# Kernel optimization log

Measured on AMD Instinct MI355X. Metric: run time of the kernel, lower is better.

## Reference

```python
import jax, jax.numpy as jnp
import numpy as np

B = 32768
N_TABLES = 26
N_ROWS = 200000
D = 64
N_DENSE = 13
NUM_PAIRS = (N_TABLES + 1) * N_TABLES // 2  # 351, pairs j < i over 27 vectors


def setup_inputs() -> dict:
    key = jax.random.key(0)
    ks = jax.random.split(key, 16)
    def lin(kw, kb, m, n):
        W = jax.random.normal(kw, (m, n), jnp.float32) * np.sqrt(2.0 / (m + n))
        b = jax.random.normal(kb, (m,), jnp.float32) * np.sqrt(1.0 / m)
        return W, b
    bw0, bb0 = lin(ks[0], ks[1], 512, N_DENSE)
    bw1, bb1 = lin(ks[2], ks[3], 256, 512)
    bw2, bb2 = lin(ks[4], ks[5], D, 256)
    tw0, tb0 = lin(ks[6], ks[7], 512, D + NUM_PAIRS)
    tw1, tb1 = lin(ks[8], ks[9], 256, 512)
    tw2, tb2 = lin(ks[10], ks[11], 1, 256)
    bound = np.sqrt(1.0 / N_ROWS)
    emb_tables = jax.random.uniform(ks[12], (N_TABLES, N_ROWS, D), jnp.float32,
                                    minval=-bound, maxval=bound)
    dense_x = jax.random.uniform(ks[13], (B, N_DENSE), jnp.float32)
    indices = jax.random.randint(ks[14], (N_TABLES, B), 0, N_ROWS, jnp.int64)
    return {"dense_x": dense_x, "indices": indices, "emb_tables": emb_tables,
            "bw0": bw0, "bb0": bb0, "bw1": bw1, "bb1": bb1, "bw2": bw2, "bb2": bb2,
            "tw0": tw0, "tb0": tb0, "tw1": tw1, "tb1": tb1, "tw2": tw2, "tb2": tb2}


def reference(dense_x, indices, emb_tables,
              bw0, bb0, bw1, bb1, bw2, bb2,
              tw0, tb0, tw1, tb1, tw2, tb2):
    # bottom MLP (all ReLU, sigmoid_bot = -1)
    h = jax.nn.relu(dense_x @ bw0.T + bb0)
    h = jax.nn.relu(h @ bw1.T + bb1)
    x_bot = jax.nn.relu(h @ bw2.T + bb2)          # [B, D]

    # multi-table EmbeddingBag(sum) with single-index bags -> plain gather
    embs = jax.vmap(lambda tbl, idx: tbl[idx])(emb_tables, indices)  # [26, B, D]

    # dot interaction over 27 feature vectors
    T = jnp.concatenate([x_bot[None], embs], axis=0).transpose(1, 0, 2)  # [B, 27, D]
    Z = jnp.einsum('bnd,bmd->bnm', T, T)                                 # [B, 27, 27]
    li, lj = jnp.tril_indices(N_TABLES + 1, k=-1)  # pairs with j < i (no self)
    Zflat = Z[:, li, lj]                           # [B, 351]
    R = jnp.concatenate([x_bot, Zflat], axis=1)    # [B, 415]

    # top MLP: ReLU, ReLU, Sigmoid (sigmoid_top = 2)
    h = jax.nn.relu(R @ tw0.T + tb0)
    h = jax.nn.relu(h @ tw1.T + tb1)
    p = jax.nn.sigmoid(h @ tw2.T + tb2)            # [B, 1]
    return p
```

## Files before the change

### kernel.cpp

```cpp
#include <hip/hip_runtime.h>
#include <cstddef>
#include <cstdint>

#define B_SZ    32768
#define NTAB    26
#define NROWS   200000

typedef __attribute__((ext_vector_type(8))) short short8v;
typedef __attribute__((ext_vector_type(4))) float f32x4;
typedef __attribute__((ext_vector_type(16))) float f32x16;

__device__ __forceinline__ ushort f2bf(float f) {
    uint32_t u = __builtin_bit_cast(uint32_t, f);
    u += 0x7FFFu + ((u >> 16) & 1u);
    return (ushort)(u >> 16);
}
__device__ __forceinline__ void stage16(const ushort* g, ushort* l) {
    __builtin_amdgcn_global_load_lds(
        (const __attribute__((address_space(1))) unsigned int*)g,
        (__attribute__((address_space(3))) unsigned int*)l, 16, 0, 0);
}

__global__ __launch_bounds__(256) void conv_all_k(
    const float* __restrict__ dense_x, const float* __restrict__ bw0,
    const float* __restrict__ tw0, const float* __restrict__ bw1,
    const float* __restrict__ bw2, const float* __restrict__ tw1,
    ushort* __restrict__ dense_pad, ushort* __restrict__ bw0p,
    ushort* __restrict__ tw0p, ushort* __restrict__ bw1c,
    ushort* __restrict__ bw2c, ushort* __restrict__ tw1c)
{
    const int gid = blockIdx.x * 256 + threadIdx.x;
    if (gid < 1048576) {
        int r = gid >> 5, k = gid & 31;
        dense_pad[gid] = (k < 13) ? f2bf(dense_x[r * 13 + k]) : (ushort)0;
    } else if (gid < 1064960) {
        int i = gid - 1048576; int r = i >> 5, k = i & 31;
        bw0p[i] = (k < 13) ? f2bf(bw0[r * 13 + k]) : (ushort)0;
    } else if (gid < 1277952) {
        int i = gid - 1064960; int r = i / 416, k = i - r * 416;
        tw0p[i] = (k < 415) ? f2bf(tw0[r * 415 + k]) : (ushort)0;
    } else if (gid < 1409024) {
        int i = gid - 1277952; bw1c[i] = f2bf(bw1[i]);
    } else if (gid < 1425408) {
        int i = gid - 1409024; bw2c[i] = f2bf(bw2[i]);
    } else if (gid < 1556480) {
        int i = gid - 1425408; tw1c[i] = f2bf(tw1[i]);
    }
}

__global__ __launch_bounds__(256, 2) void fused_k(
    const ushort* __restrict__ dense_pad, const ushort* __restrict__ bw0p,
    const float* __restrict__ bb0, const ushort* __restrict__ bw1c,
    const float* __restrict__ bb1, const ushort* __restrict__ bw2c,
    const float* __restrict__ bb2,
    const float* __restrict__ emb, const int* __restrict__ indices,
    const ushort* __restrict__ tw0p, const float* __restrict__ tb0,
    const ushort* __restrict__ tw1c, const float* __restrict__ tb1,
    const float* __restrict__ tw2, const float* __restrict__ tb2,
    float* __restrict__ out)
{
    __shared__ __align__(16) ushort R1[32 * 512];
    __shared__ __align__(16) ushort Wst[2][256 * 32];
    __shared__ __align__(16) ushort R3[32 * 256];
    const int t = threadIdx.x;
    const int lane = t & 63, w = t >> 6;
    const int fr = lane & 15, j16 = lane >> 4;
    const int bBase = blockIdx.x * 32;

    int ir0, ir1, ir2, ir3;
    ir0 = indices[(size_t)(t >> 5) * B_SZ + bBase + (t & 31)];
    ir1 = indices[(size_t)((256 + t) >> 5) * B_SZ + bBase + ((256 + t) & 31)];
    ir2 = indices[(size_t)((512 + t) >> 5) * B_SZ + bBase + ((512 + t) & 31)];
    ir3 = (t < 64) ? indices[(size_t)((768 + t) >> 5) * B_SZ + bBase + ((768 + t) & 31)] : 0;

    if (t < 128) {
        const int r = t >> 2, u = t & 3, us = u ^ ((r >> 1) & 3);
        stage16(dense_pad + (size_t)(bBase + r) * 32 + us * 8, &R3[t * 8]);
    }
#pragma unroll
    for (int i = 0; i < 4; ++i) {
        const int idx = i * 256 + t;
        const int r = idx >> 2, u = idx & 3, us = u ^ ((r >> 1) & 3);
        stage16(bw0p + (size_t)r * 32 + us * 8, &Wst[0][idx * 8]);
        stage16(bw0p + (size_t)(256 + r) * 32 + us * 8, &Wst[1][idx * 8]);
    }
    __syncthreads();

    f32x4 acc0[2][2][4] = {};
    {
        short8v a[2];
#pragma unroll
        for (int m = 0; m < 2; ++m) {
            const int r = m * 16 + fr;
            a[m] = *(const short8v*)&R3[r * 32 + (j16 ^ ((r >> 1) & 3)) * 8];
        }
#pragma unroll
        for (int hh = 0; hh < 2; ++hh) {
            short8v b[4];
#pragma unroll
            for (int n = 0; n < 4; ++n) {
                const int lr = w * 64 + n * 16 + fr;
                b[n] = *(const short8v*)&Wst[hh][lr * 32 + (j16 ^ ((lr >> 1) & 3)) * 8];
            }
            __builtin_amdgcn_s_setprio(1);
#pragma unroll
            for (int m = 0; m < 2; ++m)
#pragma unroll
                for (int n = 0; n < 4; ++n)
                    acc0[hh][m][n] = __builtin_amdgcn_mfma_f32_16x16x32_bf16(b[n], a[m], acc0[hh][m][n], 0, 0, 0);
            __builtin_amdgcn_s_setprio(0);
        }
    }
    __syncthreads();

#pragma unroll
    for (int i = 0; i < 4; ++i) {
        const int idx = i * 256 + t;
        const int r = idx >> 2, u = idx & 3, us = u ^ ((r >> 1) & 3);
        stage16(bw1c + (size_t)r * 512 + us * 8, &Wst[0][idx * 8]);
        stage16(bw1c + (size_t)r * 512 + 32 + us * 8, &Wst[1][idx * 8]);
    }
#pragma unroll
    for (int hh = 0; hh < 2; ++hh)
#pragma unroll
    for (int n = 0; n < 4; ++n) {
        const int ch = hh * 256 + w * 64 + n * 16 + j16 * 4;
        const float4 bv = *(const float4*)&bb0[ch];
#pragma unroll
        for (int m = 0; m < 2; ++m) {
            const int s = m * 16 + fr;
            ushort4 o;
            o.x = f2bf(fmaxf(acc0[hh][m][n][0] + bv.x, 0.f));
            o.y = f2bf(fmaxf(acc0[hh][m][n][1] + bv.y, 0.f));
            o.z = f2bf(fmaxf(acc0[hh][m][n][2] + bv.z, 0.f));
            o.w = f2bf(fmaxf(acc0[hh][m][n][3] + bv.w, 0.f));
            const int u = ch >> 3, su = u ^ (s & 7);
            *(ushort4*)&R1[s * 512 + su * 8 + (ch & 7)] = o;
        }
    }
    __syncthreads();

    f32x4 acc1[2][4] = {};
    for (int i8 = 0; i8 < 8; ++i8) {
#pragma unroll
        for (int half = 0; half < 2; ++half) {
            const int kt = i8 * 64 + half * 32;
            short8v a[2], b[4];
#pragma unroll
            for (int m = 0; m < 2; ++m) {
                const int s = m * 16 + fr;
                const int u = (kt >> 3) + j16, su = u ^ (s & 7);
                a[m] = *(const short8v*)&R1[s * 512 + su * 8];
            }
#pragma unroll
            for (int n = 0; n < 4; ++n) {
                const int lr = w * 64 + n * 16 + fr;
                b[n] = *(const short8v*)&Wst[half][lr * 32 + (j16 ^ ((lr >> 1) & 3)) * 8];
            }
            __builtin_amdgcn_s_setprio(1);
#pragma unroll
            for (int m = 0; m < 2; ++m)
#pragma unroll
                for (int n = 0; n < 4; ++n)
                    acc1[m][n] = __builtin_amdgcn_mfma_f32_16x16x32_bf16(b[n], a[m], acc1[m][n], 0, 0, 0);
            __builtin_amdgcn_s_setprio(0);
        }
        __syncthreads();
        if (i8 < 7) {
            const int kt2 = (i8 + 1) * 64;
#pragma unroll
            for (int i = 0; i < 4; ++i) {
                const int idx = i * 256 + t;
                const int r = idx >> 2, u = idx & 3, us = u ^ ((r >> 1) & 3);
                stage16(bw1c + (size_t)r * 512 + kt2 + us * 8, &Wst[0][idx * 8]);
                stage16(bw1c + (size_t)r * 512 + kt2 + 32 + us * 8, &Wst[1][idx * 8]);
            }
            __syncthreads();
        }
    }
    {
        const int r = t >> 2, u = t & 3, us = u ^ ((r >> 1) & 3);
        stage16(bw2c + (size_t)r * 256 + us * 8, &Wst[0][t * 8]);
        stage16(bw2c + (size_t)r * 256 + 32 + us * 8, &Wst[1][t * 8]);
    }
#pragma unroll
    for (int n = 0; n < 4; ++n) {
        const int ch = w * 64 + n * 16 + j16 * 4;
        const float4 bv = *(const float4*)&bb1[ch];
#pragma unroll
        for (int m = 0; m < 2; ++m) {
            const int s = m * 16 + fr;
            ushort4 o;
            o.x = f2bf(fmaxf(acc1[m][n][0] + bv.x, 0.f));
            o.y = f2bf(fmaxf(acc1[m][n][1] + bv.y, 0.f));
            o.z = f2bf(fmaxf(acc1[m][n][2] + bv.z, 0.f));
            o.w = f2bf(fmaxf(acc1[m][n][3] + bv.w, 0.f));
            const int u = ch >> 3, su = u ^ (s & 7);
            *(ushort4*)&R3[s * 256 + su * 8 + (ch & 7)] = o;
        }
    }
    __syncthreads();

    f32x4 acc2[2] = {};
    for (int i8 = 0; i8 < 4; ++i8) {
#pragma unroll
        for (int half = 0; half < 2; ++half) {
            const int kt = i8 * 64 + half * 32;
            short8v a[2], b;
#pragma unroll
            for (int m = 0; m < 2; ++m) {
                const int s = m * 16 + fr;
                const int u = (kt >> 3) + j16, su = u ^ (s & 7);
                a[m] = *(const short8v*)&R3[s * 256 + su * 8];
            }
            {
                const int lr = w * 16 + fr;
                b = *(const short8v*)&Wst[half][lr * 32 + (j16 ^ ((lr >> 1) & 3)) * 8];
            }
#pragma unroll
            for (int m = 0; m < 2; ++m)
                acc2[m] = __builtin_amdgcn_mfma_f32_16x16x32_bf16(b, a[m], acc2[m], 0, 0, 0);
        }
        __syncthreads();
        if (i8 < 3) {
            const int kt2 = (i8 + 1) * 64;
            const int r = t >> 2, u = t & 3, us = u ^ ((r >> 1) & 3);
            stage16(bw2c + (size_t)r * 256 + kt2 + us * 8, &Wst[0][t * 8]);
            stage16(bw2c + (size_t)r * 256 + kt2 + 32 + us * 8, &Wst[1][t * 8]);
            __syncthreads();
        }
    }
    {
        const int ch = w * 16 + j16 * 4;
        const float4 bv = *(const float4*)&bb2[ch];
#pragma unroll
        for (int m = 0; m < 2; ++m) {
            const int s = m * 16 + fr;
            ushort4 o;
            o.x = f2bf(fmaxf(acc2[m][0] + bv.x, 0.f));
            o.y = f2bf(fmaxf(acc2[m][1] + bv.y, 0.f));
            o.z = f2bf(fmaxf(acc2[m][2] + bv.z, 0.f));
            o.w = f2bf(fmaxf(acc2[m][3] + bv.w, 0.f));
            *(ushort4*)&R1[s * 424 + ch] = o;
        }
    }
    if (t < 32) R1[t * 424 + 415] = 0;
    {
        int* sc = (int*)R3;
        sc[t] = ir0; sc[256 + t] = ir1; sc[512 + t] = ir2;
        if (t < 64) sc[768 + t] = ir3;
    }
#pragma unroll
    for (int i = 0; i < 4; ++i) {
        const int idx = i * 256 + t;
        const int r = idx >> 2, u = idx & 3, us = u ^ ((r >> 1) & 3);
        stage16(tw0p + (size_t)r * 416 + us * 8, &Wst[0][idx * 8]);
        stage16(tw0p + (size_t)(256 + r) * 416 + us * 8, &Wst[1][idx * 8]);
    }
    __syncthreads();

    {
        const int* sc = (const int*)R3;
        const int r32 = lane & 31, half = lane >> 5;
        for (int it = 0; it < 8; ++it) {
            const int s = it * 4 + w;
            short8v tf[4];
            if (r32 == 0) {
#pragma unroll
                for (int kq = 0; kq < 4; ++kq)
                    tf[kq] = *(const short8v*)&R1[s * 424 + kq * 16 + half * 8];
            } else if (r32 <= 26) {
                const int idxv = sc[(r32 - 1) * 32 + s];
                const float* rp = emb + ((size_t)(r32 - 1) * NROWS + (size_t)idxv) * 64 + half * 8;
#pragma unroll
                for (int kq = 0; kq < 4; ++kq) {
                    const f32x4 x = *(const f32x4*)&rp[kq * 16];
                    const f32x4 y = *(const f32x4*)&rp[kq * 16 + 4];
                    short8v v;
                    v[0] = (short)f2bf(x[0]); v[1] = (short)f2bf(x[1]);
                    v[2] = (short)f2bf(x[2]); v[3] = (short)f2bf(x[3]);
                    v[4] = (short)f2bf(y[0]); v[5] = (short)f2bf(y[1]);
                    v[6] = (short)f2bf(y[2]); v[7] = (short)f2bf(y[3]);
                    tf[kq] = v;
                }
            } else {
#pragma unroll
                for (int kq = 0; kq < 4; ++kq) tf[kq] = (short8v)0;
            }
            f32x16 c = {};
#pragma unroll
            for (int kq = 0; kq < 4; ++kq)
                c = __builtin_amdgcn_mfma_f32_32x32x16_bf16(tf[kq], tf[kq], c, 0, 0, 0);
#pragma unroll
            for (int reg = 0; reg < 16; ++reg) {
                const int r = (reg & 3) + 8 * (reg >> 2) + 4 * half;
                if (r < 27 && r32 < r)
                    R1[s * 424 + 64 + (r * (r - 1)) / 2 + r32] = f2bf(c[reg]);
            }
        }
    }
    __syncthreads();

    f32x4 accA[2][2][4] = {};
    for (int kt_i = 0; kt_i < 13; ++kt_i) {
        const int kt = kt_i * 32;
        short8v a[2];
#pragma unroll
        for (int m = 0; m < 2; ++m) {
            const int s = m * 16 + fr;
            a[m] = *(const short8v*)&R1[s * 424 + ((kt >> 3) + j16) * 8];
        }
#pragma unroll
        for (int hh = 0; hh < 2; ++hh) {
            short8v b[4];
#pragma unroll
            for (int n = 0; n < 4; ++n) {
                const int lr = w * 64 + n * 16 + fr;
                b[n] = *(const short8v*)&Wst[hh][lr * 32 + (j16 ^ ((lr >> 1) & 3)) * 8];
            }
            __builtin_amdgcn_s_setprio(1);
#pragma unroll
            for (int m = 0; m < 2; ++m)
#pragma unroll
                for (int n = 0; n < 4; ++n)
                    accA[hh][m][n] = __builtin_amdgcn_mfma_f32_16x16x32_bf16(b[n], a[m], accA[hh][m][n], 0, 0, 0);
            __builtin_amdgcn_s_setprio(0);
        }
        __syncthreads();
        if (kt_i < 12) {
            const int kt2 = kt + 32;
#pragma unroll
            for (int i = 0; i < 4; ++i) {
                const int idx = i * 256 + t;
                const int r = idx >> 2, u = idx & 3, us = u ^ ((r >> 1) & 3);
                stage16(tw0p + (size_t)r * 416 + kt2 + us * 8, &Wst[0][idx * 8]);
                stage16(tw0p + (size_t)(256 + r) * 416 + kt2 + us * 8, &Wst[1][idx * 8]);
            }
            __syncthreads();
        }
    }
#pragma unroll
    for (int i = 0; i < 4; ++i) {
        const int idx = i * 256 + t;
        const int r = idx >> 2, u = idx & 3, us = u ^ ((r >> 1) & 3);
        stage16(tw1c + (size_t)r * 512 + us * 8, &Wst[0][idx * 8]);
        stage16(tw1c + (size_t)r * 512 + 32 + us * 8, &Wst[1][idx * 8]);
    }
#pragma unroll
    for (int hh = 0; hh < 2; ++hh)
#pragma unroll
    for (int n = 0; n < 4; ++n) {
        const int ch = hh * 256 + w * 64 + n * 16 + j16 * 4;
        const float4 bv = *(const float4*)&tb0[ch];
#pragma unroll
        for (int m = 0; m < 2; ++m) {
            const int s = m * 16 + fr;
            ushort4 o;
            o.x = f2bf(fmaxf(accA[hh][m][n][0] + bv.x, 0.f));
            o.y = f2bf(fmaxf(accA[hh][m][n][1] + bv.y, 0.f));
            o.z = f2bf(fmaxf(accA[hh][m][n][2] + bv.z, 0.f));
            o.w = f2bf(fmaxf(accA[hh][m][n][3] + bv.w, 0.f));
            const int u = ch >> 3, su = u ^ (s & 7);
            *(ushort4*)&R1[s * 512 + su * 8 + (ch & 7)] = o;
        }
    }
    __syncthreads();

    f32x4 accB[2][4] = {};
    for (int i8 = 0; i8 < 8; ++i8) {
#pragma unroll
        for (int half = 0; half < 2; ++half) {
            const int kt = i8 * 64 + half * 32;
            short8v a[2], b[4];
#pragma unroll
            for (int m = 0; m < 2; ++m) {
                const int s = m * 16 + fr;
                const int u = (kt >> 3) + j16, su = u ^ (s & 7);
                a[m] = *(const short8v*)&R1[s * 512 + su * 8];
            }
#pragma unroll
            for (int n = 0; n < 4; ++n) {
                const int lr = w * 64 + n * 16 + fr;
                b[n] = *(const short8v*)&Wst[half][lr * 32 + (j16 ^ ((lr >> 1) & 3)) * 8];
            }
            __builtin_amdgcn_s_setprio(1);
#pragma unroll
            for (int m = 0; m < 2; ++m)
#pragma unroll
                for (int n = 0; n < 4; ++n)
                    accB[m][n] = __builtin_amdgcn_mfma_f32_16x16x32_bf16(b[n], a[m], accB[m][n], 0, 0, 0);
            __builtin_amdgcn_s_setprio(0);
        }
        __syncthreads();
        if (i8 < 7) {
            const int kt2 = (i8 + 1) * 64;
#pragma unroll
            for (int i = 0; i < 4; ++i) {
                const int idx = i * 256 + t;
                const int r = idx >> 2, u = idx & 3, us = u ^ ((r >> 1) & 3);
                stage16(tw1c + (size_t)r * 512 + kt2 + us * 8, &Wst[0][idx * 8]);
                stage16(tw1c + (size_t)r * 512 + kt2 + 32 + us * 8, &Wst[1][idx * 8]);
            }
            __syncthreads();
        }
    }

    float* red = (float*)R3;
    float part[2] = {0.f, 0.f};
#pragma unroll
    for (int n = 0; n < 4; ++n) {
        const int ch = w * 64 + n * 16 + j16 * 4;
        const float4 bv = *(const float4*)&tb1[ch];
        const float4 wv = *(const float4*)&tw2[ch];
#pragma unroll
        for (int m = 0; m < 2; ++m) {
            part[m] += fmaxf(accB[m][n][0] + bv.x, 0.f) * wv.x
                     + fmaxf(accB[m][n][1] + bv.y, 0.f) * wv.y
                     + fmaxf(accB[m][n][2] + bv.z, 0.f) * wv.z
                     + fmaxf(accB[m][n][3] + bv.w, 0.f) * wv.w;
        }
    }
#pragma unroll
    for (int m = 0; m < 2; ++m) {
        float v = part[m];
        v += __shfl_xor(v, 16, 64);
        v += __shfl_xor(v, 32, 64);
        if (lane < 16) red[w * 32 + m * 16 + fr] = v;
    }
    __syncthreads();
    if (t < 32) {
        const float sm = red[t] + red[32 + t] + red[64 + t] + red[96 + t];
        out[bBase + t] = 1.f / (1.f + expf(-(sm + tb2[0])));
    }
}

extern "C" void kernel_launch(void* const* d_in, const int* in_sizes, int n_in,
                              void* d_out, int out_size, void* d_ws, size_t ws_size,
                              hipStream_t stream)
{
    (void)in_sizes; (void)n_in; (void)out_size; (void)ws_size;
    const float* dense_x = (const float*)d_in[0];
    const int*   indices = (const int*)d_in[1];
    const float* emb     = (const float*)d_in[2];
    const float* bw0 = (const float*)d_in[3];
    const float* bb0 = (const float*)d_in[4];
    const float* bw1 = (const float*)d_in[5];
    const float* bb1 = (const float*)d_in[6];
    const float* bw2 = (const float*)d_in[7];
    const float* bb2 = (const float*)d_in[8];
    const float* tw0 = (const float*)d_in[9];
    const float* tb0 = (const float*)d_in[10];
    const float* tw1 = (const float*)d_in[11];
    const float* tb1 = (const float*)d_in[12];
    const float* tw2 = (const float*)d_in[13];
    const float* tb2 = (const float*)d_in[14];
    float* out = (float*)d_out;

    ushort* ws16      = (ushort*)d_ws;
    ushort* dense_pad = ws16;
    ushort* bw0p      = dense_pad + (size_t)B_SZ * 32;
    ushort* tw0p      = bw0p + 512 * 32;
    ushort* bw1c      = tw0p + 512 * 416;
    ushort* bw2c      = bw1c + 256 * 512;
    ushort* tw1c      = bw2c + 64 * 256;

    conv_all_k<<<dim3(6080), dim3(256), 0, stream>>>(
        dense_x, bw0, tw0, bw1, bw2, tw1,
        dense_pad, bw0p, tw0p, bw1c, bw2c, tw1c);

    fused_k<<<dim3(B_SZ / 32), dim3(256), 0, stream>>>(
        dense_pad, bw0p, bb0, bw1c, bb1, bw2c, bb2,
        emb, indices, tw0p, tb0, tw1c, tb1, tw2, tb2, out);
}
```

Baseline: 112.2 us.

## Read MLP weights directly from global memory instead of staging through LDS

Removes the shared-memory weight staging buffer and its global-to-LDS copies and barriers. Every MFMA B-operand is now loaded straight from global memory (relying on L2/L1 caching), and the freed LDS allows raising the occupancy hint to 3 blocks per SM. This trades barrier and staging overhead for per-wave uncoalesced-ish global loads with latency exposed inside the MFMA loops.

```diff
diff --git a/kernel.cpp b/kernel.cpp
--- a/kernel.cpp
+++ b/kernel.cpp
@@ -48,7 +48,7 @@
     }
 }
 
-__global__ __launch_bounds__(256, 2) void fused_k(
+__global__ __launch_bounds__(256, 3) void fused_k(
     const ushort* __restrict__ dense_pad, const ushort* __restrict__ bw0p,
     const float* __restrict__ bb0, const ushort* __restrict__ bw1c,
     const float* __restrict__ bb1, const ushort* __restrict__ bw2c,
@@ -60,7 +60,6 @@
     float* __restrict__ out)
 {
     __shared__ __align__(16) ushort R1[32 * 512];
-    __shared__ __align__(16) ushort Wst[2][256 * 32];
     __shared__ __align__(16) ushort R3[32 * 256];
     const int t = threadIdx.x;
     const int lane = t & 63, w = t >> 6;
@@ -77,13 +76,6 @@
         const int r = t >> 2, u = t & 3, us = u ^ ((r >> 1) & 3);
         stage16(dense_pad + (size_t)(bBase + r) * 32 + us * 8, &R3[t * 8]);
     }
-#pragma unroll
-    for (int i = 0; i < 4; ++i) {
-        const int idx = i * 256 + t;
-        const int r = idx >> 2, u = idx & 3, us = u ^ ((r >> 1) & 3);
-        stage16(bw0p + (size_t)r * 32 + us * 8, &Wst[0][idx * 8]);
-        stage16(bw0p + (size_t)(256 + r) * 32 + us * 8, &Wst[1][idx * 8]);
-    }
     __syncthreads();
 
     f32x4 acc0[2][2][4] = {};
@@ -99,8 +91,8 @@
             short8v b[4];
 #pragma unroll
             for (int n = 0; n < 4; ++n) {
-                const int lr = w * 64 + n * 16 + fr;
-                b[n] = *(const short8v*)&Wst[hh][lr * 32 + (j16 ^ ((lr >> 1) & 3)) * 8];
+                const int lr = hh * 256 + w * 64 + n * 16 + fr;
+                b[n] = *(const short8v*)&bw0p[(size_t)lr * 32 + j16 * 8];
             }
             __builtin_amdgcn_s_setprio(1);
 #pragma unroll
@@ -110,15 +102,6 @@
                     acc0[hh][m][n] = __builtin_amdgcn_mfma_f32_16x16x32_bf16(b[n], a[m], acc0[hh][m][n], 0, 0, 0);
             __builtin_amdgcn_s_setprio(0);
         }
-    }
-    __syncthreads();
-
-#pragma unroll
-    for (int i = 0; i < 4; ++i) {
-        const int idx = i * 256 + t;
-        const int r = idx >> 2, u = idx & 3, us = u ^ ((r >> 1) & 3);
-        stage16(bw1c + (size_t)r * 512 + us * 8, &Wst[0][idx * 8]);
-        stage16(bw1c + (size_t)r * 512 + 32 + us * 8, &Wst[1][idx * 8]);
     }
 #pragma unroll
     for (int hh = 0; hh < 2; ++hh)
@@ -141,47 +124,26 @@
     __syncthreads();
 
     f32x4 acc1[2][4] = {};
-    for (int i8 = 0; i8 < 8; ++i8) {
-#pragma unroll
-        for (int half = 0; half < 2; ++half) {
-            const int kt = i8 * 64 + half * 32;
-            short8v a[2], b[4];
-#pragma unroll
-            for (int m = 0; m < 2; ++m) {
-                const int s = m * 16 + fr;
-                const int u = (kt >> 3) + j16, su = u ^ (s & 7);
-                a[m] = *(const short8v*)&R1[s * 512 + su * 8];
-            }
-#pragma unroll
-            for (int n = 0; n < 4; ++n) {
-                const int lr = w * 64 + n * 16 + fr;
-                b[n] = *(const short8v*)&Wst[half][lr * 32 + (j16 ^ ((lr >> 1) & 3)) * 8];
-            }
-            __builtin_amdgcn_s_setprio(1);
-#pragma unroll
-            for (int m = 0; m < 2; ++m)
-#pragma unroll
-                for (int n = 0; n < 4; ++n)
-                    acc1[m][n] = __builtin_amdgcn_mfma_f32_16x16x32_bf16(b[n], a[m], acc1[m][n], 0, 0, 0);
-            __builtin_amdgcn_s_setprio(0);
-        }
-        __syncthreads();
-        if (i8 < 7) {
-            const int kt2 = (i8 + 1) * 64;
-#pragma unroll
-            for (int i = 0; i < 4; ++i) {
-                const int idx = i * 256 + t;
-                const int r = idx >> 2, u = idx & 3, us = u ^ ((r >> 1) & 3);
-                stage16(bw1c + (size_t)r * 512 + kt2 + us * 8, &Wst[0][idx * 8]);
-                stage16(bw1c + (size_t)r * 512 + kt2 + 32 + us * 8, &Wst[1][idx * 8]);
-            }
-            __syncthreads();
-        }
-    }
-    {
-        const int r = t >> 2, u = t & 3, us = u ^ ((r >> 1) & 3);
-        stage16(bw2c + (size_t)r * 256 + us * 8, &Wst[0][t * 8]);
-        stage16(bw2c + (size_t)r * 256 + 32 + us * 8, &Wst[1][t * 8]);
+    for (int kt = 0; kt < 512; kt += 32) {
+        short8v a[2], b[4];
+#pragma unroll
+        for (int m = 0; m < 2; ++m) {
+            const int s = m * 16 + fr;
+            const int u = (kt >> 3) + j16, su = u ^ (s & 7);
+            a[m] = *(const short8v*)&R1[s * 512 + su * 8];
+        }
+#pragma unroll
+        for (int n = 0; n < 4; ++n) {
+            const int lr = w * 64 + n * 16 + fr;
+            b[n] = *(const short8v*)&bw1c[(size_t)lr * 512 + kt + j16 * 8];
+        }
+        __builtin_amdgcn_s_setprio(1);
+#pragma unroll
+        for (int m = 0; m < 2; ++m)
+#pragma unroll
+            for (int n = 0; n < 4; ++n)
+                acc1[m][n] = __builtin_amdgcn_mfma_f32_16x16x32_bf16(b[n], a[m], acc1[m][n], 0, 0, 0);
+        __builtin_amdgcn_s_setprio(0);
     }
 #pragma unroll
     for (int n = 0; n < 4; ++n) {
@@ -202,34 +164,24 @@
     __syncthreads();
 
     f32x4 acc2[2] = {};
-    for (int i8 = 0; i8 < 4; ++i8) {
-#pragma unroll
-        for (int half = 0; half < 2; ++half) {
-            const int kt = i8 * 64 + half * 32;
-            short8v a[2], b;
-#pragma unroll
-            for (int m = 0; m < 2; ++m) {
-                const int s = m * 16 + fr;
-                const int u = (kt >> 3) + j16, su = u ^ (s & 7);
-                a[m] = *(const short8v*)&R3[s * 256 + su * 8];
-            }
-            {
-                const int lr = w * 16 + fr;
-                b = *(const short8v*)&Wst[half][lr * 32 + (j16 ^ ((lr >> 1) & 3)) * 8];
-            }
-#pragma unroll
-            for (int m = 0; m < 2; ++m)
-                acc2[m] = __builtin_amdgcn_mfma_f32_16x16x32_bf16(b, a[m], acc2[m], 0, 0, 0);
-        }
-        __syncthreads();
-        if (i8 < 3) {
-            const int kt2 = (i8 + 1) * 64;
-            const int r = t >> 2, u = t & 3, us = u ^ ((r >> 1) & 3);
-            stage16(bw2c + (size_t)r * 256 + kt2 + us * 8, &Wst[0][t * 8]);
-            stage16(bw2c + (size_t)r * 256 + kt2 + 32 + us * 8, &Wst[1][t * 8]);
-            __syncthreads();
-        }
-    }
+    for (int kt = 0; kt < 256; kt += 32) {
+        short8v a[2], b;
+#pragma unroll
+        for (int m = 0; m < 2; ++m) {
+            const int s = m * 16 + fr;
+            const int u = (kt >> 3) + j16, su = u ^ (s & 7);
+            a[m] = *(const short8v*)&R3[s * 256 + su * 8];
+        }
+        {
+            const int lr = w * 16 + fr;
+            b = *(const short8v*)&bw2c[(size_t)lr * 256 + kt + j16 * 8];
+        }
+#pragma unroll
+        for (int m = 0; m < 2; ++m)
+            acc2[m] = __builtin_amdgcn_mfma_f32_16x16x32_bf16(b, a[m], acc2[m], 0, 0, 0);
+    }
+    __syncthreads();
+
     {
         const int ch = w * 16 + j16 * 4;
         const float4 bv = *(const float4*)&bb2[ch];
@@ -249,13 +201,6 @@
         int* sc = (int*)R3;
         sc[t] = ir0; sc[256 + t] = ir1; sc[512 + t] = ir2;
         if (t < 64) sc[768 + t] = ir3;
-    }
-#pragma unroll
-    for (int i = 0; i < 4; ++i) {
-        const int idx = i * 256 + t;
-        const int r = idx >> 2, u = idx & 3, us = u ^ ((r >> 1) & 3);
-        stage16(tw0p + (size_t)r * 416 + us * 8, &Wst[0][idx * 8]);
-        stage16(tw0p + (size_t)(256 + r) * 416 + us * 8, &Wst[1][idx * 8]);
     }
     __syncthreads();
 
@@ -302,8 +247,7 @@
     __syncthreads();
 
     f32x4 accA[2][2][4] = {};
-    for (int kt_i = 0; kt_i < 13; ++kt_i) {
-        const int kt = kt_i * 32;
+    for (int kt = 0; kt < 416; kt += 32) {
         short8v a[2];
 #pragma unroll
         for (int m = 0; m < 2; ++m) {
@@ -315,8 +259,8 @@
             short8v b[4];
 #pragma unroll
             for (int n = 0; n < 4; ++n) {
-                const int lr = w * 64 + n * 16 + fr;
-                b[n] = *(const short8v*)&Wst[hh][lr * 32 + (j16 ^ ((lr >> 1) & 3)) * 8];
+                const int lr = hh * 256 + w * 64 + n * 16 + fr;
+                b[n] = *(const short8v*)&tw0p[(size_t)lr * 416 + kt + j16 * 8];
             }
             __builtin_amdgcn_s_setprio(1);
 #pragma unroll
@@ -326,26 +270,8 @@
                     accA[hh][m][n] = __builtin_amdgcn_mfma_f32_16x16x32_bf16(b[n], a[m], accA[hh][m][n], 0, 0, 0);
             __builtin_amdgcn_s_setprio(0);
         }
-        __syncthreads();
-        if (kt_i < 12) {
-            const int kt2 = kt + 32;
-#pragma unroll
-            for (int i = 0; i < 4; ++i) {
-                const int idx = i * 256 + t;
-                const int r = idx >> 2, u = idx & 3, us = u ^ ((r >> 1) & 3);
-                stage16(tw0p + (size_t)r * 416 + kt2 + us * 8, &Wst[0][idx * 8]);
-                stage16(tw0p + (size_t)(256 + r) * 416 + kt2 + us * 8, &Wst[1][idx * 8]);
-            }
-            __syncthreads();
-        }
-    }
-#pragma unroll
-    for (int i = 0; i < 4; ++i) {
-        const int idx = i * 256 + t;
-        const int r = idx >> 2, u = idx & 3, us = u ^ ((r >> 1) & 3);
-        stage16(tw1c + (size_t)r * 512 + us * 8, &Wst[0][idx * 8]);
-        stage16(tw1c + (size_t)r * 512 + 32 + us * 8, &Wst[1][idx * 8]);
-    }
+    }
+    __syncthreads();
 #pragma unroll
     for (int hh = 0; hh < 2; ++hh)
 #pragma unroll
@@ -367,42 +293,26 @@
     __syncthreads();
 
     f32x4 accB[2][4] = {};
-    for (int i8 = 0; i8 < 8; ++i8) {
-#pragma unroll
-        for (int half = 0; half < 2; ++half) {
-            const int kt = i8 * 64 + half * 32;
-            short8v a[2], b[4];
-#pragma unroll
-            for (int m = 0; m < 2; ++m) {
-                const int s = m * 16 + fr;
-                const int u = (kt >> 3) + j16, su = u ^ (s & 7);
-                a[m] = *(const short8v*)&R1[s * 512 + su * 8];
-            }
-#pragma unroll
-            for (int n = 0; n < 4; ++n) {
-                const int lr = w * 64 + n * 16 + fr;
-                b[n] = *(const short8v*)&Wst[half][lr * 32 + (j16 ^ ((lr >> 1) & 3)) * 8];
-            }
-            __builtin_amdgcn_s_setprio(1);
-#pragma unroll
-            for (int m = 0; m < 2; ++m)
-#pragma unroll
-                for (int n = 0; n < 4; ++n)
-                    accB[m][n] = __builtin_amdgcn_mfma_f32_16x16x32_bf16(b[n], a[m], accB[m][n], 0, 0, 0);
-            __builtin_amdgcn_s_setprio(0);
-        }
-        __syncthreads();
-        if (i8 < 7) {
-            const int kt2 = (i8 + 1) * 64;
-#pragma unroll
-            for (int i = 0; i < 4; ++i) {
-                const int idx = i * 256 + t;
-                const int r = idx >> 2, u = idx & 3, us = u ^ ((r >> 1) & 3);
-                stage16(tw1c + (size_t)r * 512 + kt2 + us * 8, &Wst[0][idx * 8]);
-                stage16(tw1c + (size_t)r * 512 + kt2 + 32 + us * 8, &Wst[1][idx * 8]);
-            }
-            __syncthreads();
-        }
+    for (int kt = 0; kt < 512; kt += 32) {
+        short8v a[2], b[4];
+#pragma unroll
+        for (int m = 0; m < 2; ++m) {
+            const int s = m * 16 + fr;
+            const int u = (kt >> 3) + j16, su = u ^ (s & 7);
+            a[m] = *(const short8v*)&R1[s * 512 + su * 8];
+        }
+#pragma unroll
+        for (int n = 0; n < 4; ++n) {
+            const int lr = w * 64 + n * 16 + fr;
+            b[n] = *(const short8v*)&tw1c[(size_t)lr * 512 + kt + j16 * 8];
+        }
+        __builtin_amdgcn_s_setprio(1);
+#pragma unroll
+        for (int m = 0; m < 2; ++m)
+#pragma unroll
+            for (int n = 0; n < 4; ++n)
+                accB[m][n] = __builtin_amdgcn_mfma_f32_16x16x32_bf16(b[n], a[m], accB[m][n], 0, 0, 0);
+        __builtin_amdgcn_s_setprio(0);
     }
 
     float* red = (float*)R3;
```

Result: slower. 161.4 us (+43.9%).

## Process 64 samples per block with 8 waves to share staged weight tiles

Applied to the files above, without the earlier changes.

Each block now handles 64 batch rows using 512 threads laid out as a 2x4 wave grid (row half by column quarter) instead of 32 rows with 4 waves. Every weight tile staged into LDS is reused by twice as many samples, which halves the weight staging traffic and the number of barriers per sample. In exchange LDS use per block roughly doubles, each wave holds more accumulators in some layers, and there are half as many blocks, which can lower occupancy and latency hiding for the embedding gathers.

```diff
diff --git a/kernel.cpp b/kernel.cpp
--- a/kernel.cpp
+++ b/kernel.cpp
@@ -48,7 +48,7 @@
     }
 }
 
-__global__ __launch_bounds__(256, 2) void fused_k(
+__global__ __launch_bounds__(512, 2) void fused_k(
     const ushort* __restrict__ dense_pad, const ushort* __restrict__ bw0p,
     const float* __restrict__ bb0, const ushort* __restrict__ bw1c,
     const float* __restrict__ bb1, const ushort* __restrict__ bw2c,
@@ -59,81 +59,77 @@
     const float* __restrict__ tw2, const float* __restrict__ tb2,
     float* __restrict__ out)
 {
-    __shared__ __align__(16) ushort R1[32 * 512];
+    __shared__ __align__(16) ushort R1[64 * 512];
     __shared__ __align__(16) ushort Wst[2][256 * 32];
-    __shared__ __align__(16) ushort R3[32 * 256];
+    __shared__ __align__(16) ushort R3[64 * 256];
     const int t = threadIdx.x;
     const int lane = t & 63, w = t >> 6;
+    const int wr = w >> 2, wc = w & 3;
     const int fr = lane & 15, j16 = lane >> 4;
-    const int bBase = blockIdx.x * 32;
+    const int bBase = blockIdx.x * 64;
 
     int ir0, ir1, ir2, ir3;
-    ir0 = indices[(size_t)(t >> 5) * B_SZ + bBase + (t & 31)];
-    ir1 = indices[(size_t)((256 + t) >> 5) * B_SZ + bBase + ((256 + t) & 31)];
-    ir2 = indices[(size_t)((512 + t) >> 5) * B_SZ + bBase + ((512 + t) & 31)];
-    ir3 = (t < 64) ? indices[(size_t)((768 + t) >> 5) * B_SZ + bBase + ((768 + t) & 31)] : 0;
-
-    if (t < 128) {
+    ir0 = indices[(size_t)(t >> 6) * B_SZ + bBase + (t & 63)];
+    ir1 = indices[(size_t)((512 + t) >> 6) * B_SZ + bBase + ((512 + t) & 63)];
+    ir2 = indices[(size_t)((1024 + t) >> 6) * B_SZ + bBase + ((1024 + t) & 63)];
+    ir3 = (t < 128) ? indices[(size_t)((1536 + t) >> 6) * B_SZ + bBase + ((1536 + t) & 63)] : 0;
+
+    if (t < 256) {
         const int r = t >> 2, u = t & 3, us = u ^ ((r >> 1) & 3);
         stage16(dense_pad + (size_t)(bBase + r) * 32 + us * 8, &R3[t * 8]);
     }
 #pragma unroll
-    for (int i = 0; i < 4; ++i) {
-        const int idx = i * 256 + t;
+    for (int i = 0; i < 2; ++i) {
+        const int idx = i * 512 + t;
         const int r = idx >> 2, u = idx & 3, us = u ^ ((r >> 1) & 3);
         stage16(bw0p + (size_t)r * 32 + us * 8, &Wst[0][idx * 8]);
         stage16(bw0p + (size_t)(256 + r) * 32 + us * 8, &Wst[1][idx * 8]);
     }
     __syncthreads();
 
-    f32x4 acc0[2][2][4] = {};
+    f32x4 acc0[2][8] = {};
     {
-        short8v a[2];
-#pragma unroll
-        for (int m = 0; m < 2; ++m) {
-            const int r = m * 16 + fr;
+        short8v a[2], b[8];
+#pragma unroll
+        for (int m = 0; m < 2; ++m) {
+            const int r = wr * 32 + m * 16 + fr;
             a[m] = *(const short8v*)&R3[r * 32 + (j16 ^ ((r >> 1) & 3)) * 8];
         }
 #pragma unroll
-        for (int hh = 0; hh < 2; ++hh) {
-            short8v b[4];
-#pragma unroll
-            for (int n = 0; n < 4; ++n) {
-                const int lr = w * 64 + n * 16 + fr;
-                b[n] = *(const short8v*)&Wst[hh][lr * 32 + (j16 ^ ((lr >> 1) & 3)) * 8];
-            }
-            __builtin_amdgcn_s_setprio(1);
-#pragma unroll
-            for (int m = 0; m < 2; ++m)
-#pragma unroll
-                for (int n = 0; n < 4; ++n)
-                    acc0[hh][m][n] = __builtin_amdgcn_mfma_f32_16x16x32_bf16(b[n], a[m], acc0[hh][m][n], 0, 0, 0);
-            __builtin_amdgcn_s_setprio(0);
-        }
-    }
-    __syncthreads();
-
-#pragma unroll
-    for (int i = 0; i < 4; ++i) {
-        const int idx = i * 256 + t;
+        for (int n = 0; n < 8; ++n) {
+            const int lr = wc * 128 + n * 16 + fr;
+            const int lb = lr & 255;
+            b[n] = *(const short8v*)&Wst[lr >> 8][lb * 32 + (j16 ^ ((lb >> 1) & 3)) * 8];
+        }
+        __builtin_amdgcn_s_setprio(1);
+#pragma unroll
+        for (int m = 0; m < 2; ++m)
+#pragma unroll
+            for (int n = 0; n < 8; ++n)
+                acc0[m][n] = __builtin_amdgcn_mfma_f32_16x16x32_bf16(b[n], a[m], acc0[m][n], 0, 0, 0);
+        __builtin_amdgcn_s_setprio(0);
+    }
+    __syncthreads();
+
+#pragma unroll
+    for (int i = 0; i < 2; ++i) {
+        const int idx = i * 512 + t;
         const int r = idx >> 2, u = idx & 3, us = u ^ ((r >> 1) & 3);
         stage16(bw1c + (size_t)r * 512 + us * 8, &Wst[0][idx * 8]);
         stage16(bw1c + (size_t)r * 512 + 32 + us * 8, &Wst[1][idx * 8]);
     }
 #pragma unroll
-    for (int hh = 0; hh < 2; ++hh)
-#pragma unroll
-    for (int n = 0; n < 4; ++n) {
-        const int ch = hh * 256 + w * 64 + n * 16 + j16 * 4;
+    for (int n = 0; n < 8; ++n) {
+        const int ch = wc * 128 + n * 16 + j16 * 4;
         const float4 bv = *(const float4*)&bb0[ch];
 #pragma unroll
         for (int m = 0; m < 2; ++m) {
-            const int s = m * 16 + fr;
+            const int s = wr * 32 + m * 16 + fr;
             ushort4 o;
-            o.x = f2bf(fmaxf(acc0[hh][m][n][0] + bv.x, 0.f));
-            o.y = f2bf(fmaxf(acc0[hh][m][n][1] + bv.y, 0.f));
-            o.z = f2bf(fmaxf(acc0[hh][m][n][2] + bv.z, 0.f));
-            o.w = f2bf(fmaxf(acc0[hh][m][n][3] + bv.w, 0.f));
+            o.x = f2bf(fmaxf(acc0[m][n][0] + bv.x, 0.f));
+            o.y = f2bf(fmaxf(acc0[m][n][1] + bv.y, 0.f));
+            o.z = f2bf(fmaxf(acc0[m][n][2] + bv.z, 0.f));
+            o.w = f2bf(fmaxf(acc0[m][n][3] + bv.w, 0.f));
             const int u = ch >> 3, su = u ^ (s & 7);
             *(ushort4*)&R1[s * 512 + su * 8 + (ch & 7)] = o;
         }
@@ -148,13 +144,13 @@
             short8v a[2], b[4];
 #pragma unroll
             for (int m = 0; m < 2; ++m) {
-                const int s = m * 16 + fr;
+                const int s = wr * 32 + m * 16 + fr;
                 const int u = (kt >> 3) + j16, su = u ^ (s & 7);
                 a[m] = *(const short8v*)&R1[s * 512 + su * 8];
             }
 #pragma unroll
             for (int n = 0; n < 4; ++n) {
-                const int lr = w * 64 + n * 16 + fr;
+                const int lr = wc * 64 + n * 16 + fr;
                 b[n] = *(const short8v*)&Wst[half][lr * 32 + (j16 ^ ((lr >> 1) & 3)) * 8];
             }
             __builtin_amdgcn_s_setprio(1);
@@ -169,8 +165,8 @@
         if (i8 < 7) {
             const int kt2 = (i8 + 1) * 64;
 #pragma unroll
-            for (int i = 0; i < 4; ++i) {
-                const int idx = i * 256 + t;
+            for (int i = 0; i < 2; ++i) {
+                const int idx = i * 512 + t;
                 const int r = idx >> 2, u = idx & 3, us = u ^ ((r >> 1) & 3);
                 stage16(bw1c + (size_t)r * 512 + kt2 + us * 8, &Wst[0][idx * 8]);
                 stage16(bw1c + (size_t)r * 512 + kt2 + 32 + us * 8, &Wst[1][idx * 8]);
@@ -178,18 +174,18 @@
             __syncthreads();
         }
     }
-    {
+    if (t < 256) {
         const int r = t >> 2, u = t & 3, us = u ^ ((r >> 1) & 3);
         stage16(bw2c + (size_t)r * 256 + us * 8, &Wst[0][t * 8]);
         stage16(bw2c + (size_t)r * 256 + 32 + us * 8, &Wst[1][t * 8]);
     }
 #pragma unroll
     for (int n = 0; n < 4; ++n) {
-        const int ch = w * 64 + n * 16 + j16 * 4;
+        const int ch = wc * 64 + n * 16 + j16 * 4;
         const float4 bv = *(const float4*)&bb1[ch];
 #pragma unroll
         for (int m = 0; m < 2; ++m) {
-            const int s = m * 16 + fr;
+            const int s = wr * 32 + m * 16 + fr;
             ushort4 o;
             o.x = f2bf(fmaxf(acc1[m][n][0] + bv.x, 0.f));
             o.y = f2bf(fmaxf(acc1[m][n][1] + bv.y, 0.f));
@@ -209,12 +205,12 @@
             short8v a[2], b;
 #pragma unroll
             for (int m = 0; m < 2; ++m) {
-                const int s = m * 16 + fr;
+                const int s = wr * 32 + m * 16 + fr;
                 const int u = (kt >> 3) + j16, su = u ^ (s & 7);
                 a[m] = *(const short8v*)&R3[s * 256 + su * 8];
             }
             {
-                const int lr = w * 16 + fr;
+                const int lr = wc * 16 + fr;
                 b = *(const short8v*)&Wst[half][lr * 32 + (j16 ^ ((lr >> 1) & 3)) * 8];
             }
 #pragma unroll
@@ -224,18 +220,20 @@
         __syncthreads();
         if (i8 < 3) {
             const int kt2 = (i8 + 1) * 64;
-            const int r = t >> 2, u = t & 3, us = u ^ ((r >> 1) & 3);
-            stage16(bw2c + (size_t)r * 256 + kt2 + us * 8, &Wst[0][t * 8]);
-            stage16(bw2c + (size_t)r * 256 + kt2 + 32 + us * 8, &Wst[1][t * 8]);
+            if (t < 256) {
+                const int r = t >> 2, u = t & 3, us = u ^ ((r >> 1) & 3);
+                stage16(bw2c + (size_t)r * 256 + kt2 + us * 8, &Wst[0][t * 8]);
+                stage16(bw2c + (size_t)r * 256 + kt2 + 32 + us * 8, &Wst[1][t * 8]);
+            }
             __syncthreads();
         }
     }
     {
-        const int ch = w * 16 + j16 * 4;
+        const int ch = wc * 16 + j16 * 4;
         const float4 bv = *(const float4*)&bb2[ch];
 #pragma unroll
         for (int m = 0; m < 2; ++m) {
-            const int s = m * 16 + fr;
+            const int s = wr * 32 + m * 16 + fr;
             ushort4 o;
             o.x = f2bf(fmaxf(acc2[m][0] + bv.x, 0.f));
             o.y = f2bf(fmaxf(acc2[m][1] + bv.y, 0.f));
@@ -244,15 +242,15 @@
             *(ushort4*)&R1[s * 424 + ch] = o;
         }
     }
-    if (t < 32) R1[t * 424 + 415] = 0;
+    if (t < 64) R1[t * 424 + 415] = 0;
     {
         int* sc = (int*)R3;
-        sc[t] = ir0; sc[256 + t] = ir1; sc[512 + t] = ir2;
-        if (t < 64) sc[768 + t] = ir3;
-    }
-#pragma unroll
-    for (int i = 0; i < 4; ++i) {
-        const int idx = i * 256 + t;
+        sc[t] = ir0; sc[512 + t] = ir1; sc[1024 + t] = ir2;
+        if (t < 128) sc[1536 + t] = ir3;
+    }
+#pragma unroll
+    for (int i = 0; i < 2; ++i) {
+        const int idx = i * 512 + t;
         const int r = idx >> 2, u = idx & 3, us = u ^ ((r >> 1) & 3);
         stage16(tw0p + (size_t)r * 416 + us * 8, &Wst[0][idx * 8]);
         stage16(tw0p + (size_t)(256 + r) * 416 + us * 8, &Wst[1][idx * 8]);
@@ -263,14 +261,14 @@
         const int* sc = (const int*)R3;
         const int r32 = lane & 31, half = lane >> 5;
         for (int it = 0; it < 8; ++it) {
-            const int s = it * 4 + w;
+            const int s = it * 8 + w;
             short8v tf[4];
             if (r32 == 0) {
 #pragma unroll
                 for (int kq = 0; kq < 4; ++kq)
                     tf[kq] = *(const short8v*)&R1[s * 424 + kq * 16 + half * 8];
             } else if (r32 <= 26) {
-                const int idxv = sc[(r32 - 1) * 32 + s];
+                const int idxv = sc[(r32 - 1) * 64 + s];
                 const float* rp = emb + ((size_t)(r32 - 1) * NROWS + (size_t)idxv) * 64 + half * 8;
 #pragma unroll
                 for (int kq = 0; kq < 4; ++kq) {
@@ -301,37 +299,34 @@
     }
     __syncthreads();
 
-    f32x4 accA[2][2][4] = {};
+    f32x4 accA[2][8] = {};
     for (int kt_i = 0; kt_i < 13; ++kt_i) {
         const int kt = kt_i * 32;
-        short8v a[2];
-#pragma unroll
-        for (int m = 0; m < 2; ++m) {
-            const int s = m * 16 + fr;
+        short8v a[2], b[8];
+#pragma unroll
+        for (int m = 0; m < 2; ++m) {
+            const int s = wr * 32 + m * 16 + fr;
             a[m] = *(const short8v*)&R1[s * 424 + ((kt >> 3) + j16) * 8];
         }
 #pragma unroll
-        for (int hh = 0; hh < 2; ++hh) {
-            short8v b[4];
-#pragma unroll
-            for (int n = 0; n < 4; ++n) {
-                const int lr = w * 64 + n * 16 + fr;
-                b[n] = *(const short8v*)&Wst[hh][lr * 32 + (j16 ^ ((lr >> 1) & 3)) * 8];
-            }
-            __builtin_amdgcn_s_setprio(1);
-#pragma unroll
-            for (int m = 0; m < 2; ++m)
-#pragma unroll
-                for (int n = 0; n < 4; ++n)
-                    accA[hh][m][n] = __builtin_amdgcn_mfma_f32_16x16x32_bf16(b[n], a[m], accA[hh][m][n], 0, 0, 0);
-            __builtin_amdgcn_s_setprio(0);
-        }
+        for (int n = 0; n < 8; ++n) {
+            const int lr = wc * 128 + n * 16 + fr;
+            const int lb = lr & 255;
+            b[n] = *(const short8v*)&Wst[lr >> 8][lb * 32 + (j16 ^ ((lb >> 1) & 3)) * 8];
+        }
+        __builtin_amdgcn_s_setprio(1);
+#pragma unroll
+        for (int m = 0; m < 2; ++m)
+#pragma unroll
+            for (int n = 0; n < 8; ++n)
+                accA[m][n] = __builtin_amdgcn_mfma_f32_16x16x32_bf16(b[n], a[m], accA[m][n], 0, 0, 0);
+        __builtin_amdgcn_s_setprio(0);
         __syncthreads();
         if (kt_i < 12) {
             const int kt2 = kt + 32;
 #pragma unroll
-            for (int i = 0; i < 4; ++i) {
-                const int idx = i * 256 + t;
+            for (int i = 0; i < 2; ++i) {
+                const int idx = i * 512 + t;
                 const int r = idx >> 2, u = idx & 3, us = u ^ ((r >> 1) & 3);
                 stage16(tw0p + (size_t)r * 416 + kt2 + us * 8, &Wst[0][idx * 8]);
                 stage16(tw0p + (size_t)(256 + r) * 416 + kt2 + us * 8, &Wst[1][idx * 8]);
@@ -340,26 +335,24 @@
         }
     }
 #pragma unroll
-    for (int i = 0; i < 4; ++i) {
-        const int idx = i * 256 + t;
+    for (int i = 0; i < 2; ++i) {
+        const int idx = i * 512 + t;
         const int r = idx >> 2, u = idx & 3, us = u ^ ((r >> 1) & 3);
         stage16(tw1c + (size_t)r * 512 + us * 8, &Wst[0][idx * 8]);
         stage16(tw1c + (size_t)r * 512 + 32 + us * 8, &Wst[1][idx * 8]);
     }
 #pragma unroll
-    for (int hh = 0; hh < 2; ++hh)
-#pragma unroll
-    for (int n = 0; n < 4; ++n) {
-        const int ch = hh * 256 + w * 64 + n * 16 + j16 * 4;
+    for (int n = 0; n < 8; ++n) {
+        const int ch = wc * 128 + n * 16 + j16 * 4;
         const float4 bv = *(const float4*)&tb0[ch];
 #pragma unroll
         for (int m = 0; m < 2; ++m) {
-            const int s = m * 16 + fr;
+            const int s = wr * 32 + m * 16 + fr;
             ushort4 o;
-            o.x = f2bf(fmaxf(accA[hh][m][n][0] + bv.x, 0.f));
-            o.y = f2bf(fmaxf(accA[hh][m][n][1] + bv.y, 0.f));
-            o.z = f2bf(fmaxf(accA[hh][m][n][2] + bv.z, 0.f));
-            o.w = f2bf(fmaxf(accA[hh][m][n][3] + bv.w, 0.f));
+            o.x = f2bf(fmaxf(accA[m][n][0] + bv.x, 0.f));
+            o.y = f2bf(fmaxf(accA[m][n][1] + bv.y, 0.f));
+            o.z = f2bf(fmaxf(accA[m][n][2] + bv.z, 0.f));
+            o.w = f2bf(fmaxf(accA[m][n][3] + bv.w, 0.f));
             const int u = ch >> 3, su = u ^ (s & 7);
             *(ushort4*)&R1[s * 512 + su * 8 + (ch & 7)] = o;
         }
@@ -374,13 +367,13 @@
             short8v a[2], b[4];
 #pragma unroll
             for (int m = 0; m < 2; ++m) {
-                const int s = m * 16 + fr;
+                const int s = wr * 32 + m * 16 + fr;
                 const int u = (kt >> 3) + j16, su = u ^ (s & 7);
                 a[m] = *(const short8v*)&R1[s * 512 + su * 8];
             }
 #pragma unroll
             for (int n = 0; n < 4; ++n) {
-                const int lr = w * 64 + n * 16 + fr;
+                const int lr = wc * 64 + n * 16 + fr;
                 b[n] = *(const short8v*)&Wst[half][lr * 32 + (j16 ^ ((lr >> 1) & 3)) * 8];
             }
             __builtin_amdgcn_s_setprio(1);
@@ -395,8 +388,8 @@
         if (i8 < 7) {
             const int kt2 = (i8 + 1) * 64;
 #pragma unroll
-            for (int i = 0; i < 4; ++i) {
-                const int idx = i * 256 + t;
+            for (int i = 0; i < 2; ++i) {
+                const int idx = i * 512 + t;
                 const int r = idx >> 2, u = idx & 3, us = u ^ ((r >> 1) & 3);
                 stage16(tw1c + (size_t)r * 512 + kt2 + us * 8, &Wst[0][idx * 8]);
                 stage16(tw1c + (size_t)r * 512 + kt2 + 32 + us * 8, &Wst[1][idx * 8]);
@@ -409,7 +402,7 @@
     float part[2] = {0.f, 0.f};
 #pragma unroll
     for (int n = 0; n < 4; ++n) {
-        const int ch = w * 64 + n * 16 + j16 * 4;
+        const int ch = wc * 64 + n * 16 + j16 * 4;
         const float4 bv = *(const float4*)&tb1[ch];
         const float4 wv = *(const float4*)&tw2[ch];
 #pragma unroll
@@ -425,11 +418,11 @@
         float v = part[m];
         v += __shfl_xor(v, 16, 64);
         v += __shfl_xor(v, 32, 64);
-        if (lane < 16) red[w * 32 + m * 16 + fr] = v;
-    }
-    __syncthreads();
-    if (t < 32) {
-        const float sm = red[t] + red[32 + t] + red[64 + t] + red[96 + t];
+        if (lane < 16) red[wc * 64 + wr * 32 + m * 16 + fr] = v;
+    }
+    __syncthreads();
+    if (t < 64) {
+        const float sm = red[t] + red[64 + t] + red[128 + t] + red[192 + t];
         out[bBase + t] = 1.f / (1.f + expf(-(sm + tb2[0])));
     }
 }
@@ -468,7 +461,7 @@
         dense_x, bw0, tw0, bw1, bw2, tw1,
         dense_pad, bw0p, tw0p, bw1c, bw2c, tw1c);
 
-    fused_k<<<dim3(B_SZ / 32), dim3(256), 0, stream>>>(
+    fused_k<<<dim3(B_SZ / 64), dim3(512), 0, stream>>>(
         dense_pad, bw0p, bb0, bw1c, bb1, bw2c, bb2,
         emb, indices, tw0p, tb0, tw1c, tb1, tw2, tb2, out);
 }
```

New measurement: 116.4 us. 1.04x slower.

## Stage full bw2 in LDS and software-pipeline embedding gathers with double buffering

Applied to the files above, without the earlier changes.

Loads all of bw2 into the combined LDS staging buffer in one shot, so the layer-3 loop runs without repeated restaging and barriers. The tw0 staging is issued earlier so it overlaps the bias epilogue. The embedding interaction loop is double-buffered: the raw fp32 rows for the next sample are fetched while the current sample is converted and run through MFMA, hiding gather latency. Keeping two sets of eight f32x4 buffers live raises register pressure, which could hurt occupancy at launch_bounds(256,2). Rows that are not embeddings (the dense row and the padding rows) now load from a clamped address and the loaded value is discarded.

```diff
diff --git a/kernel.cpp b/kernel.cpp
--- a/kernel.cpp
+++ b/kernel.cpp
@@ -62,6 +62,7 @@
     __shared__ __align__(16) ushort R1[32 * 512];
     __shared__ __align__(16) ushort Wst[2][256 * 32];
     __shared__ __align__(16) ushort R3[32 * 256];
+    ushort* const Wf = &Wst[0][0];
     const int t = threadIdx.x;
     const int lane = t & 63, w = t >> 6;
     const int fr = lane & 15, j16 = lane >> 4;
@@ -178,10 +179,12 @@
             __syncthreads();
         }
     }
-    {
-        const int r = t >> 2, u = t & 3, us = u ^ ((r >> 1) & 3);
-        stage16(bw2c + (size_t)r * 256 + us * 8, &Wst[0][t * 8]);
-        stage16(bw2c + (size_t)r * 256 + 32 + us * 8, &Wst[1][t * 8]);
+#pragma unroll
+    for (int i = 0; i < 8; ++i) {
+        const int idx = i * 256 + t;
+        const int st = idx >> 8, within = idx & 255;
+        const int r = within >> 2, u = within & 3, us = u ^ ((r >> 1) & 3);
+        stage16(bw2c + (size_t)r * 256 + st * 32 + us * 8, &Wf[idx * 8]);
     }
 #pragma unroll
     for (int n = 0; n < 4; ++n) {
@@ -202,33 +205,30 @@
     __syncthreads();
 
     f32x4 acc2[2] = {};
-    for (int i8 = 0; i8 < 4; ++i8) {
-#pragma unroll
-        for (int half = 0; half < 2; ++half) {
-            const int kt = i8 * 64 + half * 32;
-            short8v a[2], b;
-#pragma unroll
-            for (int m = 0; m < 2; ++m) {
-                const int s = m * 16 + fr;
-                const int u = (kt >> 3) + j16, su = u ^ (s & 7);
-                a[m] = *(const short8v*)&R3[s * 256 + su * 8];
-            }
-            {
-                const int lr = w * 16 + fr;
-                b = *(const short8v*)&Wst[half][lr * 32 + (j16 ^ ((lr >> 1) & 3)) * 8];
-            }
-#pragma unroll
-            for (int m = 0; m < 2; ++m)
-                acc2[m] = __builtin_amdgcn_mfma_f32_16x16x32_bf16(b, a[m], acc2[m], 0, 0, 0);
-        }
-        __syncthreads();
-        if (i8 < 3) {
-            const int kt2 = (i8 + 1) * 64;
-            const int r = t >> 2, u = t & 3, us = u ^ ((r >> 1) & 3);
-            stage16(bw2c + (size_t)r * 256 + kt2 + us * 8, &Wst[0][t * 8]);
-            stage16(bw2c + (size_t)r * 256 + kt2 + 32 + us * 8, &Wst[1][t * 8]);
-            __syncthreads();
-        }
+    for (int kt = 0; kt < 256; kt += 32) {
+        short8v a[2], b;
+#pragma unroll
+        for (int m = 0; m < 2; ++m) {
+            const int s = m * 16 + fr;
+            const int u = (kt >> 3) + j16, su = u ^ (s & 7);
+            a[m] = *(const short8v*)&R3[s * 256 + su * 8];
+        }
+        {
+            const int lr = w * 16 + fr;
+            b = *(const short8v*)&Wf[(kt >> 5) * 2048 + lr * 32 + (j16 ^ ((lr >> 1) & 3)) * 8];
+        }
+#pragma unroll
+        for (int m = 0; m < 2; ++m)
+            acc2[m] = __builtin_amdgcn_mfma_f32_16x16x32_bf16(b, a[m], acc2[m], 0, 0, 0);
+    }
+    __syncthreads();
+
+#pragma unroll
+    for (int i = 0; i < 4; ++i) {
+        const int idx = i * 256 + t;
+        const int r = idx >> 2, u = idx & 3, us = u ^ ((r >> 1) & 3);
+        stage16(tw0p + (size_t)r * 416 + us * 8, &Wst[0][idx * 8]);
+        stage16(tw0p + (size_t)(256 + r) * 416 + us * 8, &Wst[1][idx * 8]);
     }
     {
         const int ch = w * 16 + j16 * 4;
@@ -250,54 +250,57 @@
         sc[t] = ir0; sc[256 + t] = ir1; sc[512 + t] = ir2;
         if (t < 64) sc[768 + t] = ir3;
     }
-#pragma unroll
-    for (int i = 0; i < 4; ++i) {
-        const int idx = i * 256 + t;
-        const int r = idx >> 2, u = idx & 3, us = u ^ ((r >> 1) & 3);
-        stage16(tw0p + (size_t)r * 416 + us * 8, &Wst[0][idx * 8]);
-        stage16(tw0p + (size_t)(256 + r) * 416 + us * 8, &Wst[1][idx * 8]);
-    }
     __syncthreads();
 
     {
         const int* sc = (const int*)R3;
         const int r32 = lane & 31, half = lane >> 5;
-        for (int it = 0; it < 8; ++it) {
-            const int s = it * 4 + w;
-            short8v tf[4];
-            if (r32 == 0) {
-#pragma unroll
-                for (int kq = 0; kq < 4; ++kq)
-                    tf[kq] = *(const short8v*)&R1[s * 424 + kq * 16 + half * 8];
-            } else if (r32 <= 26) {
-                const int idxv = sc[(r32 - 1) * 32 + s];
-                const float* rp = emb + ((size_t)(r32 - 1) * NROWS + (size_t)idxv) * 64 + half * 8;
-#pragma unroll
-                for (int kq = 0; kq < 4; ++kq) {
-                    const f32x4 x = *(const f32x4*)&rp[kq * 16];
-                    const f32x4 y = *(const f32x4*)&rp[kq * 16 + 4];
-                    short8v v;
-                    v[0] = (short)f2bf(x[0]); v[1] = (short)f2bf(x[1]);
-                    v[2] = (short)f2bf(x[2]); v[3] = (short)f2bf(x[3]);
-                    v[4] = (short)f2bf(y[0]); v[5] = (short)f2bf(y[1]);
-                    v[6] = (short)f2bf(y[2]); v[7] = (short)f2bf(y[3]);
-                    tf[kq] = v;
-                }
-            } else {
-#pragma unroll
-                for (int kq = 0; kq < 4; ++kq) tf[kq] = (short8v)0;
-            }
-            f32x16 c = {};
-#pragma unroll
-            for (int kq = 0; kq < 4; ++kq)
-                c = __builtin_amdgcn_mfma_f32_32x32x16_bf16(tf[kq], tf[kq], c, 0, 0, 0);
-#pragma unroll
-            for (int reg = 0; reg < 16; ++reg) {
-                const int r = (reg & 3) + 8 * (reg >> 2) + 4 * half;
-                if (r < 27 && r32 < r)
-                    R1[s * 424 + 64 + (r * (r - 1)) / 2 + r32] = f2bf(c[reg]);
-            }
-        }
+        const bool isEmb = (r32 >= 1) && (r32 <= 26);
+        const size_t tblOfs = isEmb ? (size_t)(r32 - 1) * NROWS : 0;
+
+#define LOADRAW(dst, s_) { \
+        const int idxv = isEmb ? sc[(r32 - 1) * 32 + (s_)] : 0; \
+        const float* rp = emb + (tblOfs + (size_t)idxv) * 64 + half * 8; \
+        _Pragma("unroll") \
+        for (int kq = 0; kq < 4; ++kq) { \
+            dst[2 * kq]     = *(const f32x4*)&rp[kq * 16]; \
+            dst[2 * kq + 1] = *(const f32x4*)&rp[kq * 16 + 4]; } }
+
+#define COMPUTE(raw, s_) { \
+        short8v tf[4]; \
+        _Pragma("unroll") \
+        for (int kq = 0; kq < 4; ++kq) { \
+            short8v v; \
+            v[0] = (short)f2bf(raw[2 * kq][0]);     v[1] = (short)f2bf(raw[2 * kq][1]); \
+            v[2] = (short)f2bf(raw[2 * kq][2]);     v[3] = (short)f2bf(raw[2 * kq][3]); \
+            v[4] = (short)f2bf(raw[2 * kq + 1][0]); v[5] = (short)f2bf(raw[2 * kq + 1][1]); \
+            v[6] = (short)f2bf(raw[2 * kq + 1][2]); v[7] = (short)f2bf(raw[2 * kq + 1][3]); \
+            if (r32 == 0) v = *(const short8v*)&R1[(s_) * 424 + kq * 16 + half * 8]; \
+            else if (!isEmb) v = (short8v)0; \
+            tf[kq] = v; } \
+        f32x16 c = {}; \
+        _Pragma("unroll") \
+        for (int kq = 0; kq < 4; ++kq) \
+            c = __builtin_amdgcn_mfma_f32_32x32x16_bf16(tf[kq], tf[kq], c, 0, 0, 0); \
+        _Pragma("unroll") \
+        for (int reg = 0; reg < 16; ++reg) { \
+            const int r = (reg & 3) + 8 * (reg >> 2) + 4 * half; \
+            if (r < 27 && r32 < r) \
+                R1[(s_) * 424 + 64 + (r * (r - 1)) / 2 + r32] = f2bf(c[reg]); } }
+
+        f32x4 rawA[8], rawB[8];
+        LOADRAW(rawA, w);
+#pragma unroll
+        for (int p = 0; p < 4; ++p) {
+            const int sA = p * 8 + w;
+            const int sB = p * 8 + 4 + w;
+            LOADRAW(rawB, sB);
+            COMPUTE(rawA, sA);
+            if (p < 3) LOADRAW(rawA, p * 8 + 8 + w);
+            COMPUTE(rawB, sB);
+        }
+#undef LOADRAW
+#undef COMPUTE
     }
     __syncthreads();
 
```

Result: faster. 108.7 us, median of 2 (-3.1%).
